# Kernel optimization log

Measured on AMD Instinct MI355X. Metric: run time of the kernel, lower is better.

Reference implementation:

```python
import jax, jax.numpy as jnp
import numpy as np

N = 50000       # nodes
E_RAND = 800000 # random edges (avg degree ~16)
K = 64          # edges touching `node`; setup_inputs guarantees exactly K
F = 64          # num_node_features
C = 64          # conv_channels


def setup_inputs() -> dict:
    key = jax.random.key(0)
    ks = jax.random.split(key, 6)
    x = jax.random.normal(ks[0], (N, F), dtype=jnp.float32)
    # random edges avoiding node 0 so exactly the K prepended edges touch node 0
    src = jax.random.randint(ks[1], (E_RAND,), 1, N, dtype=jnp.int64)
    dst = jax.random.randint(ks[2], (E_RAND,), 1, N, dtype=jnp.int64)
    ksrc = jnp.zeros((K,), dtype=jnp.int64)
    kdst = jnp.arange(1, K + 1, dtype=jnp.int64)
    edge_index = jnp.stack([jnp.concatenate([ksrc, src]),
                            jnp.concatenate([kdst, dst])])  # [2, K+E_RAND]
    W1 = jax.random.normal(ks[3], (F, C), jnp.float32) / np.float32(np.sqrt(F))
    b1 = jnp.zeros((C,), jnp.float32)
    W2 = jax.random.normal(ks[4], (C, C), jnp.float32) / np.float32(np.sqrt(C))
    b2 = jnp.zeros((C,), jnp.float32)
    Wr = jax.random.normal(ks[5], (C, 1), jnp.float32) / np.float32(np.sqrt(C))
    br = jnp.zeros((1,), jnp.float32)
    return {"x": x, "edge_index": edge_index, "node": 0,
            "W1": W1, "b1": b1, "W2": W2, "b2": b2, "Wr": Wr, "br": br}


def gcn_conv(x, src, dst, W, b):
    """PyG GCNConv with self-loops already appended to (src, dst).
    out[v] = sum_{(u,v)} deg(u)^-1/2 * deg(v)^-1/2 * (x @ W)[u] + b
    """
    n = x.shape[0]
    xw = x @ W                                              # [N, C]
    deg = jnp.zeros((n,), xw.dtype).at[dst].add(1.0)        # in-degree incl. self-loop
    dinv = jnp.where(deg > 0, jax.lax.rsqrt(deg), 0.0)
    norm = dinv[src] * dinv[dst]                            # [E]
    out = jax.ops.segment_sum(xw[src] * norm[:, None], dst, num_segments=n)
    return out + b


def reference(x, edge_index, node, W1, b1, W2, b2, Wr, br):
    n = x.shape[0]
    loop = jnp.arange(n, dtype=edge_index.dtype)
    src = jnp.concatenate([edge_index[0], loop])  # add self loops (GCNConv default)
    dst = jnp.concatenate([edge_index[1], loop])
    h = jax.nn.relu(gcn_conv(x, src, dst, W1, b1))
    h = jax.nn.relu(gcn_conv(h, src, dst, W2, b2))
    # edges incident to `node` (setup guarantees exactly K such edges)
    s0, d0 = edge_index[0], edge_index[1]
    mask = (s0 == node) | (d0 == node)
    idx = jnp.nonzero(mask, size=K)[0]
    s, d = s0[idx], d0[idx]
    targets = jnp.where(s == node, d, s)  # self-loop (s==d==node) -> node
    score = h[targets] @ Wr + br          # [K, 1]
    score = jax.nn.softmax(score, axis=0)
    return score[:, 0], targets
```

## Files before the change

### kernel.cpp

```cpp
#include <hip/hip_runtime.h>
#include <math.h>

#define KK 64
#define CAP 64
#define NF 4160
#define BMW 1568

__global__ __launch_bounds__(256) void k_find(const int* __restrict__ ei, int E,
                                              const int* __restrict__ nodep,
                                              int4* __restrict__ zbase, int zcount4,
                                              int* __restrict__ tcount,
                                              int* __restrict__ tpairs) {
    int idx = blockIdx.x * 256 + threadIdx.x;
    if (idx < zcount4) zbase[idx] = make_int4(0, 0, 0, 0);
    int node = nodep[0];
    int n4 = E >> 2;
    if (idx < n4) {
        int4 ss = ((const int4*)ei)[idx];
        int4 dd = ((const int4*)(ei + E))[idx];
        int s[4] = {ss.x, ss.y, ss.z, ss.w};
        int d[4] = {dd.x, dd.y, dd.z, dd.w};
#pragma unroll
        for (int k = 0; k < 4; k++) {
            if (s[k] == node || d[k] == node) {
                int q = atomicAdd(tcount, 1);
                if (q < KK) { int e = idx * 4 + k; tpairs[2 * q] = e; tpairs[2 * q + 1] = (s[k] == node) ? d[k] : s[k]; }
            }
        }
    }
    if (idx == 0) {
        for (int e = n4 * 4; e < E; e++) {
            int s = ei[e], d = ei[E + e];
            if (s == node || d == node) {
                int q = atomicAdd(tcount, 1);
                if (q < KK) { tpairs[2 * q] = e; tpairs[2 * q + 1] = (s == node) ? d : s; }
            }
        }
    }
}

__global__ __launch_bounds__(256) void k_collect_t(const int* __restrict__ ei, int E,
                                                   const int* __restrict__ tpairs,
                                                   int* __restrict__ cnt,
                                                   int* __restrict__ tcnt2,
                                                   int* __restrict__ tslots,
                                                   int* __restrict__ fmapRow,
                                                   int* __restrict__ tsorted_g,
                                                   int* __restrict__ towner_g) {
    __shared__ unsigned int bmask[BMW];
    __shared__ int tnode[KK];
    __shared__ int eidx[KK], tgt[KK], srt[KK];
    int tid = threadIdx.x;
    for (int i = tid; i < BMW; i += 256) bmask[i] = 0u;
    if (tid < KK) { eidx[tid] = tpairs[2 * tid]; tgt[tid] = tpairs[2 * tid + 1]; }
    __syncthreads();
    if (tid < KK) {
        int rank = 0;
        for (int j = 0; j < KK; j++) rank += (eidx[j] < eidx[tid]) ? 1 : 0;
        srt[rank] = tgt[tid];
    }
    __syncthreads();
    if (tid < KK) {
        int mynode = srt[tid];
        int owner = tid;
        for (int j = 0; j < tid; j++) if (srt[j] == mynode) { owner = j; break; }
        tnode[tid] = (owner == tid) ? mynode : -1;
        if (owner == tid) atomicOr(&bmask[mynode >> 5], 1u << (mynode & 31));
        if (blockIdx.x == 0) {
            tsorted_g[tid] = mynode; towner_g[tid] = owner;
            if (owner == tid) atomicCAS(&fmapRow[mynode], 0, tid * 65 + 0 + 1);
        }
    }
    __syncthreads();
    int n4 = E >> 2;
    for (int idx = blockIdx.x * 256 + tid; idx < n4; idx += gridDim.x * 256) {
        int4 ss = ((const int4*)ei)[idx];
        int4 dd = ((const int4*)(ei + E))[idx];
        int s[4] = {ss.x, ss.y, ss.z, ss.w};
        int d[4] = {dd.x, dd.y, dd.z, dd.w};
        atomicAdd(&cnt[d[0]], 1);
        atomicAdd(&cnt[d[1]], 1);
#pragma unroll
        for (int k = 0; k < 4; k++) {
            if ((bmask[d[k] >> 5] >> (d[k] & 31)) & 1u) {
                int f = 0;
                for (int j = 0; j < KK; j++) if (tnode[j] == d[k]) { f = j + 1; break; }
                if (f) {
                    int p = atomicAdd(&tcnt2[f - 1], 1);
                    if (p < CAP) {
                        tslots[(f - 1) * CAP + p] = s[k];
                        atomicCAS(&fmapRow[s[k]], 0, (f - 1) * 65 + (p + 1) + 1);
                    }
                }
            }
        }
    }
    if (blockIdx.x == 0 && tid == 0) {
        for (int e = n4 * 4; e < E; e++) {
            int d = ei[E + e];
            atomicAdd(&cnt[d], 1);
            if ((bmask[d >> 5] >> (d & 31)) & 1u) {
                int f = 0;
                for (int j = 0; j < KK; j++) if (tnode[j] == d) { f = j + 1; break; }
                if (f) {
                    int p = atomicAdd(&tcnt2[f - 1], 1);
                    if (p < CAP) {
                        tslots[(f - 1) * CAP + p] = ei[e];
                        atomicCAS(&fmapRow[ei[e]], 0, (f - 1) * 65 + (p + 1) + 1);
                    }
                }
            }
        }
    }
}

__device__ __forceinline__ int fnode_of(int i, const int* tsorted, const int* towner,
                                        const int* tcnt2, const int* tslots) {
    int tp = i / 65, j = i % 65;
    if (j == 0) return tsorted[tp];
    int own = towner[tp];
    int c = tcnt2[own]; if (c > CAP) c = CAP;
    return (j - 1 < c) ? tslots[own * CAP + (j - 1)] : -1;
}

__global__ __launch_bounds__(256) void k_collect_f(const int* __restrict__ ei, int E,
                                                   const int* __restrict__ fmapRow,
                                                   int* __restrict__ cnt,
                                                   int* __restrict__ fcnt,
                                                   int* __restrict__ fslots) {
    int idx = blockIdx.x * 256 + threadIdx.x;
    int n4 = E >> 2;
    if (idx < n4) {
        int4 ss = ((const int4*)ei)[idx];
        int4 dd = ((const int4*)(ei + E))[idx];
        int s[4] = {ss.x, ss.y, ss.z, ss.w};
        int d[4] = {dd.x, dd.y, dd.z, dd.w};
        atomicAdd(&cnt[d[2]], 1);
        atomicAdd(&cnt[d[3]], 1);
        int r0 = fmapRow[d[0]], r1 = fmapRow[d[1]], r2 = fmapRow[d[2]], r3 = fmapRow[d[3]];
        if (r0) { int p = atomicAdd(&fcnt[r0 - 1], 1); if (p < CAP) fslots[(size_t)(r0 - 1) * CAP + p] = s[0]; }
        if (r1) { int p = atomicAdd(&fcnt[r1 - 1], 1); if (p < CAP) fslots[(size_t)(r1 - 1) * CAP + p] = s[1]; }
        if (r2) { int p = atomicAdd(&fcnt[r2 - 1], 1); if (p < CAP) fslots[(size_t)(r2 - 1) * CAP + p] = s[2]; }
        if (r3) { int p = atomicAdd(&fcnt[r3 - 1], 1); if (p < CAP) fslots[(size_t)(r3 - 1) * CAP + p] = s[3]; }
    }
    if (idx == 0) {
        for (int e = n4 * 4; e < E; e++) {
            int r = fmapRow[ei[E + e]];
            if (r) { int p = atomicAdd(&fcnt[r - 1], 1); if (p < CAP) fslots[(size_t)(r - 1) * CAP + p] = ei[e]; }
        }
    }
}

__global__ __launch_bounds__(256) void k_layer1(const float* __restrict__ x,
                                                const int* __restrict__ tsorted,
                                                const int* __restrict__ towner,
                                                const int* __restrict__ tcnt2,
                                                const int* __restrict__ tslots,
                                                const int* __restrict__ fmapRow,
                                                const int* __restrict__ cnt,
                                                const int* __restrict__ fcnt,
                                                const int* __restrict__ fslots,
                                                const float* __restrict__ W1,
                                                const float* __restrict__ b1,
                                                float* __restrict__ h1s) {
    __shared__ __align__(16) float W1s[64 * 64];
    __shared__ int anyown;
    int tid = threadIdx.x;
    int i = blockIdx.x * 4 + (tid >> 6);
    int lane = tid & 63;
    int u = -1, own = 0;
    if (i < NF) {
        u = fnode_of(i, tsorted, towner, tcnt2, tslots);
        if (u >= 0) own = (fmapRow[u] == i + 1);
    }
    if (tid == 0) anyown = 0;
    __syncthreads();
    if (lane == 0 && own) anyown = 1;
    __syncthreads();
    if (!anyown) return;
    for (int j = tid; j < 1024; j += 256) ((float4*)W1s)[j] = ((const float4*)W1)[j];
    __syncthreads();
    if (!own) return;
    float du = rsqrtf((float)(cnt[u] + 1));
    float acc = du * x[(size_t)u * 64 + lane];
    int c = fcnt[i]; if (c > CAP) c = CAP;
    const int* sl = fslots + (size_t)i * CAP;
    int k = 0;
    for (; k + 4 <= c; k += 4) {
        int u0 = sl[k], u1 = sl[k + 1], u2 = sl[k + 2], u3 = sl[k + 3];
        float f0 = rsqrtf((float)(cnt[u0] + 1));
        float f1 = rsqrtf((float)(cnt[u1] + 1));
        float f2 = rsqrtf((float)(cnt[u2] + 1));
        float f3 = rsqrtf((float)(cnt[u3] + 1));
        acc += f0 * x[(size_t)u0 * 64 + lane] + f1 * x[(size_t)u1 * 64 + lane]
             + f2 * x[(size_t)u2 * 64 + lane] + f3 * x[(size_t)u3 * 64 + lane];
    }
    for (; k < c; k++) {
        int uu = sl[k];
        acc += rsqrtf((float)(cnt[uu] + 1)) * x[(size_t)uu * 64 + lane];
    }
    float z = du * acc;
    float h = 0.f;
#pragma unroll
    for (int f = 0; f < 64; f++) h += __shfl(z, f) * W1s[f * 64 + lane];
    h = fmaxf(h + b1[lane], 0.f);
    h1s[(size_t)i * 64 + lane] = du * h;
}

__global__ __launch_bounds__(64) void k_score2(const float* __restrict__ h1s,
                                               const int* __restrict__ tsorted,
                                               const int* __restrict__ towner,
                                               const int* __restrict__ tcnt2,
                                               const int* __restrict__ tslots,
                                               const int* __restrict__ fmapRow,
                                               const int* __restrict__ cnt,
                                               const float* __restrict__ W2,
                                               const float* __restrict__ b2,
                                               const float* __restrict__ Wr,
                                               float* __restrict__ sc) {
    int tp = blockIdx.x;
    int lane = threadIdx.x;
    int t = tsorted[tp];
    float dt = rsqrtf((float)(cnt[t] + 1));
    int own = towner[tp];
    int c = tcnt2[own]; if (c > CAP) c = CAP;
    const int* sl = tslots + own * CAP;
    float z = h1s[(size_t)(fmapRow[t] - 1) * 64 + lane];
#pragma unroll 8
    for (int j = 0; j < c; j++) {
        int u = sl[j];
        int row = fmapRow[u] - 1;
        z += h1s[(size_t)row * 64 + lane];
    }
    z *= dt;
    float acc = 0.f;
#pragma unroll
    for (int f = 0; f < 64; f++) acc += __shfl(z, f) * W2[f * 64 + lane];
    float h2 = fmaxf(acc + b2[lane], 0.f);
    float p = h2 * Wr[lane];
#pragma unroll
    for (int off = 32; off >= 1; off >>= 1) p += __shfl_xor(p, off);
    if (lane == 0) sc[tp] = p;
}

__global__ void k_softmax(const float* __restrict__ sc, const int* __restrict__ tsorted,
                          float* __restrict__ out) {
    int t = threadIdx.x;
    float s = sc[t];
    float m = s;
#pragma unroll
    for (int off = 32; off >= 1; off >>= 1) m = fmaxf(m, __shfl_xor(m, off));
    float e = __expf(s - m);
    float ss = e;
#pragma unroll
    for (int off = 32; off >= 1; off >>= 1) ss += __shfl_xor(ss, off);
    out[t] = e / ss;
    out[KK + t] = (float)tsorted[t];
}

extern "C" void kernel_launch(void* const* d_in, const int* in_sizes, int n_in,
                              void* d_out, int out_size, void* d_ws, size_t ws_size,
                              hipStream_t stream) {
    const float* x  = (const float*)d_in[0];
    const int*   ei = (const int*)d_in[1];
    const int*   nodep = (const int*)d_in[2];
    const float* W1 = (const float*)d_in[3];
    const float* b1 = (const float*)d_in[4];
    const float* W2 = (const float*)d_in[5];
    const float* b2 = (const float*)d_in[6];
    const float* Wr = (const float*)d_in[7];
    const float* br = (const float*)d_in[8];
    float* out = (float*)d_out;
    (void)br;

    int N = in_sizes[0] / 64;
    int E = in_sizes[1] / 2;

    char* w = (char*)d_ws;
    int* cnt     = (int*)w; w += (size_t)N * 4;
    int* fmapRow = (int*)w; w += (size_t)N * 4;
    int* fcnt    = (int*)w; w += (size_t)NF * 4;
    int* tcnt2   = (int*)w; w += KK * 4;
    int zcount4 = (2 * N + NF + KK) / 4;
    int* tcount = (int*)w; w += 16;
    int* tpairs  = (int*)w; w += 2 * KK * 4;
    int* tsorted = (int*)w; w += KK * 4;
    int* towner  = (int*)w; w += KK * 4;
    int* tslots  = (int*)w; w += (size_t)KK * CAP * 4;
    int* fslots  = (int*)w; w += (size_t)NF * CAP * 4;
    float* h1s   = (float*)w; w += (size_t)NF * 64 * 4;
    float* sc    = (float*)w; w += KK * 4;

    hipMemsetAsync(tcount, 0, 16, stream);

    int n4 = E >> 2;
    int ebl = (n4 + 255) / 256;
    k_find<<<ebl, 256, 0, stream>>>(ei, E, nodep, (int4*)cnt, zcount4, tcount, tpairs);
    k_collect_t<<<512, 256, 0, stream>>>(ei, E, tpairs, cnt, tcnt2, tslots, fmapRow, tsorted, towner);
    k_collect_f<<<ebl, 256, 0, stream>>>(ei, E, fmapRow, cnt, fcnt, fslots);
    k_layer1<<<(NF + 3) / 4, 256, 0, stream>>>(x, tsorted, towner, tcnt2, tslots, fmapRow,
                                               cnt, fcnt, fslots, W1, b1, h1s);
    k_score2<<<KK, 64, 0, stream>>>(h1s, tsorted, towner, tcnt2, tslots, fmapRow,
                                    cnt, W2, b2, Wr, sc);
    k_softmax<<<1, 64, 0, stream>>>(sc, tsorted, out);
}
```

Before: 148.4 us.

## Compact owner rows into a list, grid-stride layer1, fuse softmax into score kernel

k_collect_f now also builds a compacted list of (row, node) owner pairs through an atomic counter. k_layer1 then runs a fixed 288-block grid-stride loop over only those pairs, instead of launching one block per four candidate rows and exiting most of them. The separate softmax kernel is removed: the last k_score2 block, detected with an atomic done counter and release/acquire ordering, computes the softmax. This saves one launch and the wasted blocks, at the cost of extra atomics and a serial dependency on the last block.

Measured after the change: 145.7 us. No clear change (-1.8%).

```diff
diff --git a/kernel.cpp b/kernel.cpp
--- a/kernel.cpp
+++ b/kernel.cpp
@@ -5,6 +5,15 @@
 #define CAP 64
 #define NF 4160
 #define BMW 1568
+
+__device__ __forceinline__ int fnode_of(int i, const int* tsorted, const int* towner,
+                                        const int* tcnt2, const int* tslots) {
+    int tp = i / 65, j = i % 65;
+    if (j == 0) return tsorted[tp];
+    int own = towner[tp];
+    int c = tcnt2[own]; if (c > CAP) c = CAP;
+    return (j - 1 < c) ? tslots[own * CAP + (j - 1)] : -1;
+}
 
 __global__ __launch_bounds__(256) void k_find(const int* __restrict__ ei, int E,
                                               const int* __restrict__ nodep,
@@ -114,34 +123,36 @@
     }
 }
 
-__device__ __forceinline__ int fnode_of(int i, const int* tsorted, const int* towner,
-                                        const int* tcnt2, const int* tslots) {
-    int tp = i / 65, j = i % 65;
-    if (j == 0) return tsorted[tp];
-    int own = towner[tp];
-    int c = tcnt2[own]; if (c > CAP) c = CAP;
-    return (j - 1 < c) ? tslots[own * CAP + (j - 1)] : -1;
-}
-
 __global__ __launch_bounds__(256) void k_collect_f(const int* __restrict__ ei, int E,
                                                    const int* __restrict__ fmapRow,
                                                    int* __restrict__ cnt,
                                                    int* __restrict__ fcnt,
-                                                   int* __restrict__ fslots) {
+                                                   int* __restrict__ fslots,
+                                                   const int* __restrict__ tsorted,
+                                                   const int* __restrict__ towner,
+                                                   const int* __restrict__ tcnt2,
+                                                   const int* __restrict__ tslots,
+                                                   int* __restrict__ ownerCount,
+                                                   int2* __restrict__ owners) {
     int idx = blockIdx.x * 256 + threadIdx.x;
+    if (idx < NF) {
+        int u = fnode_of(idx, tsorted, towner, tcnt2, tslots);
+        if (u >= 0 && fmapRow[u] == idx + 1) {
+            int p = atomicAdd(ownerCount, 1);
+            owners[p] = make_int2(idx, u);
+        }
+    }
     int n4 = E >> 2;
     if (idx < n4) {
         int4 ss = ((const int4*)ei)[idx];
         int4 dd = ((const int4*)(ei + E))[idx];
-        int s[4] = {ss.x, ss.y, ss.z, ss.w};
-        int d[4] = {dd.x, dd.y, dd.z, dd.w};
-        atomicAdd(&cnt[d[2]], 1);
-        atomicAdd(&cnt[d[3]], 1);
-        int r0 = fmapRow[d[0]], r1 = fmapRow[d[1]], r2 = fmapRow[d[2]], r3 = fmapRow[d[3]];
-        if (r0) { int p = atomicAdd(&fcnt[r0 - 1], 1); if (p < CAP) fslots[(size_t)(r0 - 1) * CAP + p] = s[0]; }
-        if (r1) { int p = atomicAdd(&fcnt[r1 - 1], 1); if (p < CAP) fslots[(size_t)(r1 - 1) * CAP + p] = s[1]; }
-        if (r2) { int p = atomicAdd(&fcnt[r2 - 1], 1); if (p < CAP) fslots[(size_t)(r2 - 1) * CAP + p] = s[2]; }
-        if (r3) { int p = atomicAdd(&fcnt[r3 - 1], 1); if (p < CAP) fslots[(size_t)(r3 - 1) * CAP + p] = s[3]; }
+        atomicAdd(&cnt[dd.z], 1);
+        atomicAdd(&cnt[dd.w], 1);
+        int r0 = fmapRow[dd.x], r1 = fmapRow[dd.y], r2 = fmapRow[dd.z], r3 = fmapRow[dd.w];
+        if (r0) { int p = atomicAdd(&fcnt[r0 - 1], 1); if (p < CAP) fslots[(size_t)(r0 - 1) * CAP + p] = ss.x; }
+        if (r1) { int p = atomicAdd(&fcnt[r1 - 1], 1); if (p < CAP) fslots[(size_t)(r1 - 1) * CAP + p] = ss.y; }
+        if (r2) { int p = atomicAdd(&fcnt[r2 - 1], 1); if (p < CAP) fslots[(size_t)(r2 - 1) * CAP + p] = ss.z; }
+        if (r3) { int p = atomicAdd(&fcnt[r3 - 1], 1); if (p < CAP) fslots[(size_t)(r3 - 1) * CAP + p] = ss.w; }
     }
     if (idx == 0) {
         for (int e = n4 * 4; e < E; e++) {
@@ -152,11 +163,8 @@
 }
 
 __global__ __launch_bounds__(256) void k_layer1(const float* __restrict__ x,
-                                                const int* __restrict__ tsorted,
-                                                const int* __restrict__ towner,
-                                                const int* __restrict__ tcnt2,
-                                                const int* __restrict__ tslots,
-                                                const int* __restrict__ fmapRow,
+                                                const int2* __restrict__ owners,
+                                                const int* __restrict__ ownerCount,
                                                 const int* __restrict__ cnt,
                                                 const int* __restrict__ fcnt,
                                                 const int* __restrict__ fslots,
@@ -164,47 +172,43 @@
                                                 const float* __restrict__ b1,
                                                 float* __restrict__ h1s) {
     __shared__ __align__(16) float W1s[64 * 64];
-    __shared__ int anyown;
     int tid = threadIdx.x;
-    int i = blockIdx.x * 4 + (tid >> 6);
-    int lane = tid & 63;
-    int u = -1, own = 0;
-    if (i < NF) {
-        u = fnode_of(i, tsorted, towner, tcnt2, tslots);
-        if (u >= 0) own = (fmapRow[u] == i + 1);
-    }
-    if (tid == 0) anyown = 0;
-    __syncthreads();
-    if (lane == 0 && own) anyown = 1;
-    __syncthreads();
-    if (!anyown) return;
+    int nown = ownerCount[0];
+    int ngrp = (nown + 3) >> 2;
+    if ((int)blockIdx.x >= ngrp) return;
     for (int j = tid; j < 1024; j += 256) ((float4*)W1s)[j] = ((const float4*)W1)[j];
     __syncthreads();
-    if (!own) return;
-    float du = rsqrtf((float)(cnt[u] + 1));
-    float acc = du * x[(size_t)u * 64 + lane];
-    int c = fcnt[i]; if (c > CAP) c = CAP;
-    const int* sl = fslots + (size_t)i * CAP;
-    int k = 0;
-    for (; k + 4 <= c; k += 4) {
-        int u0 = sl[k], u1 = sl[k + 1], u2 = sl[k + 2], u3 = sl[k + 3];
-        float f0 = rsqrtf((float)(cnt[u0] + 1));
-        float f1 = rsqrtf((float)(cnt[u1] + 1));
-        float f2 = rsqrtf((float)(cnt[u2] + 1));
-        float f3 = rsqrtf((float)(cnt[u3] + 1));
-        acc += f0 * x[(size_t)u0 * 64 + lane] + f1 * x[(size_t)u1 * 64 + lane]
-             + f2 * x[(size_t)u2 * 64 + lane] + f3 * x[(size_t)u3 * 64 + lane];
-    }
-    for (; k < c; k++) {
-        int uu = sl[k];
-        acc += rsqrtf((float)(cnt[uu] + 1)) * x[(size_t)uu * 64 + lane];
-    }
-    float z = du * acc;
-    float h = 0.f;
-#pragma unroll
-    for (int f = 0; f < 64; f++) h += __shfl(z, f) * W1s[f * 64 + lane];
-    h = fmaxf(h + b1[lane], 0.f);
-    h1s[(size_t)i * 64 + lane] = du * h;
+    int lane = tid & 63;
+    for (int g = blockIdx.x; g < ngrp; g += gridDim.x) {
+        int idx = g * 4 + (tid >> 6);
+        if (idx >= nown) continue;
+        int2 ou = owners[idx];
+        int i = ou.x, u = ou.y;
+        float du = rsqrtf((float)(cnt[u] + 1));
+        float acc = du * x[(size_t)u * 64 + lane];
+        int c = fcnt[i]; if (c > CAP) c = CAP;
+        const int* sl = fslots + (size_t)i * CAP;
+        int k = 0;
+        for (; k + 4 <= c; k += 4) {
+            int u0 = sl[k], u1 = sl[k + 1], u2 = sl[k + 2], u3 = sl[k + 3];
+            float f0 = rsqrtf((float)(cnt[u0] + 1));
+            float f1 = rsqrtf((float)(cnt[u1] + 1));
+            float f2 = rsqrtf((float)(cnt[u2] + 1));
+            float f3 = rsqrtf((float)(cnt[u3] + 1));
+            acc += f0 * x[(size_t)u0 * 64 + lane] + f1 * x[(size_t)u1 * 64 + lane]
+                 + f2 * x[(size_t)u2 * 64 + lane] + f3 * x[(size_t)u3 * 64 + lane];
+        }
+        for (; k < c; k++) {
+            int uu = sl[k];
+            acc += rsqrtf((float)(cnt[uu] + 1)) * x[(size_t)uu * 64 + lane];
+        }
+        float z = du * acc;
+        float h = 0.f;
+#pragma unroll
+        for (int f = 0; f < 64; f++) h += __shfl(z, f) * W1s[f * 64 + lane];
+        h = fmaxf(h + b1[lane], 0.f);
+        h1s[(size_t)i * 64 + lane] = du * h;
+    }
 }
 
 __global__ __launch_bounds__(64) void k_score2(const float* __restrict__ h1s,
@@ -217,7 +221,9 @@
                                                const float* __restrict__ W2,
                                                const float* __restrict__ b2,
                                                const float* __restrict__ Wr,
-                                               float* __restrict__ sc) {
+                                               float* __restrict__ sc,
+                                               int* __restrict__ done,
+                                               float* __restrict__ out) {
     int tp = blockIdx.x;
     int lane = threadIdx.x;
     int t = tsorted[tp];
@@ -240,22 +246,24 @@
     float p = h2 * Wr[lane];
 #pragma unroll
     for (int off = 32; off >= 1; off >>= 1) p += __shfl_xor(p, off);
-    if (lane == 0) sc[tp] = p;
-}
-
-__global__ void k_softmax(const float* __restrict__ sc, const int* __restrict__ tsorted,
-                          float* __restrict__ out) {
-    int t = threadIdx.x;
-    float s = sc[t];
-    float m = s;
-#pragma unroll
-    for (int off = 32; off >= 1; off >>= 1) m = fmaxf(m, __shfl_xor(m, off));
-    float e = __expf(s - m);
-    float ss = e;
-#pragma unroll
-    for (int off = 32; off >= 1; off >>= 1) ss += __shfl_xor(ss, off);
-    out[t] = e / ss;
-    out[KK + t] = (float)tsorted[t];
+    int last = 0;
+    if (lane == 0) {
+        __hip_atomic_store(&sc[tp], p, __ATOMIC_RELEASE, __HIP_MEMORY_SCOPE_AGENT);
+        last = (__hip_atomic_fetch_add(done, 1, __ATOMIC_ACQ_REL, __HIP_MEMORY_SCOPE_AGENT) == KK - 1) ? 1 : 0;
+    }
+    last = __shfl(last, 0);
+    if (last) {
+        float s = __hip_atomic_load(&sc[lane], __ATOMIC_ACQUIRE, __HIP_MEMORY_SCOPE_AGENT);
+        float m = s;
+#pragma unroll
+        for (int off = 32; off >= 1; off >>= 1) m = fmaxf(m, __shfl_xor(m, off));
+        float e = __expf(s - m);
+        float ssum = e;
+#pragma unroll
+        for (int off = 32; off >= 1; off >>= 1) ssum += __shfl_xor(ssum, off);
+        out[lane] = e / ssum;
+        out[KK + lane] = (float)tsorted[lane];
+    }
 }
 
 extern "C" void kernel_launch(void* const* d_in, const int* in_sizes, int n_in,
@@ -271,7 +279,7 @@
     const float* Wr = (const float*)d_in[7];
     const float* br = (const float*)d_in[8];
     float* out = (float*)d_out;
-    (void)br;
+    (void)br; (void)n_in; (void)out_size; (void)ws_size;
 
     int N = in_sizes[0] / 64;
     int E = in_sizes[1] / 2;
@@ -281,12 +289,14 @@
     int* fmapRow = (int*)w; w += (size_t)N * 4;
     int* fcnt    = (int*)w; w += (size_t)NF * 4;
     int* tcnt2   = (int*)w; w += KK * 4;
-    int zcount4 = (2 * N + NF + KK) / 4;
+    int* aux     = (int*)w; w += 16;
+    int zcount4 = (2 * N + NF + KK + 4) / 4;
     int* tcount = (int*)w; w += 16;
     int* tpairs  = (int*)w; w += 2 * KK * 4;
     int* tsorted = (int*)w; w += KK * 4;
     int* towner  = (int*)w; w += KK * 4;
     int* tslots  = (int*)w; w += (size_t)KK * CAP * 4;
+    int2* owners = (int2*)w; w += (size_t)NF * 8;
     int* fslots  = (int*)w; w += (size_t)NF * CAP * 4;
     float* h1s   = (float*)w; w += (size_t)NF * 64 * 4;
     float* sc    = (float*)w; w += KK * 4;
@@ -297,10 +307,9 @@
     int ebl = (n4 + 255) / 256;
     k_find<<<ebl, 256, 0, stream>>>(ei, E, nodep, (int4*)cnt, zcount4, tcount, tpairs);
     k_collect_t<<<512, 256, 0, stream>>>(ei, E, tpairs, cnt, tcnt2, tslots, fmapRow, tsorted, towner);
-    k_collect_f<<<ebl, 256, 0, stream>>>(ei, E, fmapRow, cnt, fcnt, fslots);
-    k_layer1<<<(NF + 3) / 4, 256, 0, stream>>>(x, tsorted, towner, tcnt2, tslots, fmapRow,
-                                               cnt, fcnt, fslots, W1, b1, h1s);
+    k_collect_f<<<ebl, 256, 0, stream>>>(ei, E, fmapRow, cnt, fcnt, fslots,
+                                         tsorted, towner, tcnt2, tslots, &aux[0], owners);
+    k_layer1<<<288, 256, 0, stream>>>(x, owners, &aux[0], cnt, fcnt, fslots, W1, b1, h1s);
     k_score2<<<KK, 64, 0, stream>>>(h1s, tsorted, towner, tcnt2, tslots, fmapRow,
-                                    cnt, W2, b2, Wr, sc);
-    k_softmax<<<1, 64, 0, stream>>>(sc, tsorted, out);
-}
+                                    cnt, W2, b2, Wr, sc, &aux[1], out);
+}
```
